# Optimization experiments

Measured on AMD Instinct MI355X. Metric: run time of the kernel, lower is better.

The kernel has to match this reference:

```python
import jax, jax.numpy as jnp
import numpy as np

N_NODES = 100000
N_EDGES = 3200000
D_FEAT = 128
K = 10
A_PARAM = 0.5
B_PARAM = 0.5
LMAX = 2.0


def setup_inputs() -> dict:
    key = jax.random.key(0)
    k1, k2, k3, k4 = jax.random.split(key, 4)
    x = jax.random.normal(k1, (N_NODES, D_FEAT), dtype=jnp.float32)
    edge_index = jax.random.randint(k2, (2, N_EDGES), 0, N_NODES, dtype=jnp.int32)
    alpha = jax.random.uniform(k3, (K + 1,), minval=0.9, maxval=1.1, dtype=jnp.float32)
    beta = jax.random.uniform(k4, (K + 1,), minval=0.9, maxval=1.1, dtype=jnp.float32)
    gamma = jnp.full((K,), 0.1, dtype=jnp.float32)
    return {"x": x, "alpha": alpha, "beta": beta, "gamma": gamma, "edge_index": edge_index}


def reference(x, alpha, beta, gamma, edge_index):
    n = x.shape[0]
    row, col = edge_index[0], edge_index[1]
    # sym-normalized Laplacian L = I - D^{-1/2} A D^{-1/2} (PyG get_laplacian)
    w = jnp.ones(row.shape[0], dtype=x.dtype)
    deg = jax.ops.segment_sum(w, row, num_segments=n)
    dis = jnp.where(deg > 0, jax.lax.rsqrt(jnp.maximum(deg, 1e-30)), 0.0)
    norm = dis[row] * dis[col]  # [E] edge weights of normalized adjacency

    def L_scaled_mm(y):
        # (2/lmax) * L @ y - y, with L @ y = y - Ahat @ y
        ahat_y = jax.ops.segment_sum(norm[:, None] * y[col], row, num_segments=n)
        return (2.0 / LMAX) * (y - ahat_y) - y

    a, b = A_PARAM, B_PARAM
    P_prev2 = x  # P_0
    out = alpha[0] * x
    gamma_prod = jnp.asarray(1.0, dtype=x.dtype)

    if K >= 1:
        P_prev1 = (a - b) / 2.0 * x + (a + b + 2.0) / 2.0 * L_scaled_mm(x)  # P_1
        gamma_prod = gamma_prod * gamma[0]
        out = out + beta[1] * gamma_prod * P_prev1

    for k in range(2, K + 1):
        theta = (2 * k + a + b) * (2 * k + a + b - 1) / (2 * k * (k + a + b))
        theta_p = (2 * k + a + b - 1) * (a ** 2 - b ** 2) / (
            2 * k * (k + a + b) * (2 * k + a + b - 2))
        theta_pp = (k + a - 1) * (k + b - 1) * (2 * k + a + b) / (
            k * (k + a + b) * (2 * k + a + b - 2))
        P_k = theta * L_scaled_mm(P_prev1) + theta_p * P_prev1 - theta_pp * P_prev2
        gamma_prod = gamma_prod * gamma[k - 1]
        out = out + beta[k] * gamma_prod * P_k
        P_prev2, P_prev1 = P_prev1, P_k

    return out
```

## Files before the change

kernel.cpp:

```cpp
#include <hip/hip_runtime.h>

#define NN 100000
#define NE 3200000
#define D 128
#define ND (NN * D)
#define KMAX 10
#define RPB 4
#define RBLK ((NN + RPB - 1) / RPB)
#define NEPAD (NE + 8 * NN + 128)
#define SKIP_EPS 1e-3f
#define NBUCK ((NN + 127) / 128)
#define CH 8192
#define NCB ((NE + CH - 1) / CH)

typedef float f32x4 __attribute__((ext_vector_type(4)));

__device__ __forceinline__ float bflo(unsigned u) { return __uint_as_float(u << 16); }
__device__ __forceinline__ float bfhi(unsigned u) { return __uint_as_float(u & 0xffff0000u); }
__device__ __forceinline__ unsigned packbf(float lo, float hi) {
    unsigned bx = __float_as_uint(lo);
    bx = (bx + 0x7fffu + ((bx >> 16) & 1u)) >> 16;
    unsigned by = __float_as_uint(hi);
    by = (by + 0x7fffu + ((by >> 16) & 1u)) & 0xffff0000u;
    return by | bx;
}

__global__ __launch_bounds__(256) void hist_kernel(const int* __restrict__ row,
                                                   int* __restrict__ hist) {
    __shared__ int lh[NBUCK];
    int t = threadIdx.x;
    for (int b = t; b < NBUCK; b += 256) lh[b] = 0;
    __syncthreads();
    int e0 = blockIdx.x * CH;
    int n = NE - e0; if (n > CH) n = CH;
    for (int i = t; i < n; i += 256)
        atomicAdd(&lh[row[e0 + i] >> 7], 1);
    __syncthreads();
    int x = blockIdx.x & 7;
    for (int b = t; b < NBUCK; b += 256)
        if (lh[b]) atomicAdd(&hist[x * NBUCK + b], lh[b]);
}

__global__ __launch_bounds__(1024) void scan_small_kernel(
    const int* __restrict__ hist, int* __restrict__ seg_off,
    int* __restrict__ cnt2, int* __restrict__ bbase, int* __restrict__ ebase,
    const float* __restrict__ alpha, const float* __restrict__ beta,
    const float* __restrict__ gamma, int* __restrict__ skipflag,
    float* __restrict__ fcoef, int* __restrict__ meta,
    float* __restrict__ dis) {
    __shared__ int sA[1024], sB[1024];
    int t = threadIdx.x;
    int tot = 0;
    int so[8];
    if (t < NBUCK) {
        int s = 0;
        for (int x = 0; x < 8; ++x) { so[x] = s; s += hist[x * NBUCK + t]; }
        tot = s;
    }
    int reg = (t < NBUCK) ? ((tot + 896 + 7) & ~7) : 0;
    sA[t] = tot; sB[t] = reg;
    __syncthreads();
    for (int off = 1; off < 1024; off <<= 1) {
        int a = (t >= off) ? sA[t - off] : 0;
        int c = (t >= off) ? sB[t - off] : 0;
        __syncthreads();
        sA[t] += a; sB[t] += c;
        __syncthreads();
    }
    if (t < NBUCK) {
        int ba = sA[t] - tot, eb = sB[t] - reg;
        bbase[t] = ba; ebase[t] = eb;
        for (int x = 0; x < 8; ++x) {
            seg_off[x * NBUCK + t] = ba + so[x];
            cnt2[x * NBUCK + t] = 0;
        }
    }
    if (t == 0) {
        bbase[NBUCK] = sA[1023];
        ebase[NBUCK] = sB[1023];
        dis[NN] = 0.0f;
        float g[KMAX];
        for (int i = 0; i < KMAX; ++i) g[i] = gamma[i];
        float bt[KMAX + 1];
        for (int j = 0; j <= KMAX; ++j) bt[j] = beta[j];
        fcoef[0] = alpha[0];
        float gp = 1.0f;
        skipflag[0] = 0;
        for (int k = 1; k <= KMAX; ++k) {
            gp *= g[k - 1];
            fcoef[k] = bt[k] * gp;
            float gl = 1.0f;
            for (int i = 0; i < k; ++i) gl *= fabsf(g[i]);
            float rem = 0.0f;
            for (int j = k; j <= KMAX; ++j) {
                rem = fmaxf(rem, fabsf(bt[j]) * gl);
                if (j < KMAX) gl *= fabsf(g[j - 1]);
            }
            skipflag[k] = (rem < SKIP_EPS) ? 1 : 0;
        }
        int L = 1;
        for (int k = 1; k <= KMAX; ++k) if (!skipflag[k]) L = k;
        meta[0] = L;
    }
}

__global__ __launch_bounds__(256) void bin_kernel(const int* __restrict__ row,
                                                  const int* __restrict__ col,
                                                  const int* __restrict__ seg_off,
                                                  int* __restrict__ cnt2,
                                                  int* __restrict__ bin) {
    __shared__ unsigned sval[CH];
    __shared__ unsigned short sbuck[CH];
    __shared__ int lhist[NBUCK], lpos[NBUCK], lbase[NBUCK];
    int t = threadIdx.x;
    for (int b = t; b < NBUCK; b += 256) { lhist[b] = 0; lpos[b] = 0; }
    __syncthreads();
    int e0 = blockIdx.x * CH;
    int n = NE - e0; if (n > CH) n = CH;
    for (int i = t; i < n; i += 256) {
        int r = row[e0 + i], c = col[e0 + i];
        int b = r >> 7;
        sval[i] = ((unsigned)(r & 127) << 17) | (unsigned)c;
        sbuck[i] = (unsigned short)b;
        atomicAdd(&lhist[b], 1);
    }
    __syncthreads();
    int x = blockIdx.x & 7;
    for (int b = t; b < NBUCK; b += 256)
        if (lhist[b]) lbase[b] = seg_off[x * NBUCK + b] +
                                 atomicAdd(&cnt2[x * NBUCK + b], lhist[b]);
    __syncthreads();
    for (int i = t; i < n; i += 256) {
        int b = sbuck[i];
        int p = atomicAdd(&lpos[b], 1);
        bin[lbase[b] + p] = sval[i];
    }
}

__global__ __launch_bounds__(256) void csr_fill_kernel(const int* __restrict__ bbase,
                                                       const int* __restrict__ ebase,
                                                       const int* __restrict__ bin,
                                                       int* __restrict__ ecol,
                                                       int* __restrict__ rowptr,
                                                       int* __restrict__ degp,
                                                       float* __restrict__ dis) {
    __shared__ int cnt[128], rb[128], sscan[128];
    int b = blockIdx.x, t = threadIdx.x;
    int r0 = b << 7;
    int nrows = NN - r0; if (nrows > 128) nrows = 128;
    if (t < 128) cnt[t] = 0;
    __syncthreads();
    int bb = bbase[b], be = bbase[b + 1];
    for (int i = bb + t; i < be; i += 256)
        atomicAdd(&cnt[((unsigned)bin[i]) >> 17], 1);
    __syncthreads();
    int d = 0, d8 = 0;
    if (t < 128) { d = cnt[t]; d8 = (d + 7) & ~7; sscan[t] = d8; }
    __syncthreads();
    for (int off = 1; off < 128; off <<= 1) {
        int v = 0;
        if (t < 128 && t >= off) v = sscan[t - off];
        __syncthreads();
        if (t < 128) sscan[t] += v;
        __syncthreads();
    }
    int eb0 = ebase[b];
    if (t < 128) {
        rb[t] = eb0 + sscan[t] - d8;
        if (t < nrows) {
            rowptr[r0 + t] = rb[t];
            degp[r0 + t] = d8;
            dis[r0 + t] = d > 0 ? rsqrtf((float)d) : 0.0f;
        }
        cnt[t] = 0;
    }
    __syncthreads();
    for (int i = bb + t; i < be; i += 256) {
        unsigned e = (unsigned)bin[i];
        int rl = e >> 17;
        int c = e & 0x1FFFF;
        int p = atomicAdd(&cnt[rl], 1);
        ecol[rb[rl] + p] = c;
    }
    __syncthreads();
    for (int i = t; i < nrows * 8; i += 256) {
        int rl = i >> 3, j = i & 7;
        int dd = cnt[rl];
        if (dd + j < ((dd + 7) & ~7)) ecol[rb[rl] + dd + j] = NN;
    }
}

__global__ __launch_bounds__(256) void ewt_kernel(int* __restrict__ ecol,
                                                  const float* __restrict__ dis,
                                                  float* __restrict__ ewt) {
    int i = blockIdx.x * 256 + threadIdx.x;
    if (i >= NEPAD) return;
    unsigned c = (unsigned)ecol[i];
    unsigned cc = c < NN ? c : NN;
    ewt[i] = dis[cc];
    ecol[i] = (int)((c < NN ? c : 0u) << 8);
}

__global__ __launch_bounds__(256) void x2bf_kernel(const float2* __restrict__ x,
                                                   unsigned* __restrict__ xb) {
    int i = blockIdx.x * 256 + threadIdx.x;
    if (i >= ND / 2) return;
    float2 v = x[i];
    xb[i] = packbf(v.x, v.y);
}

#define FMA8(U, W)                                               \
    a0 = fmaf(W, bflo(U.x), a0); a1 = fmaf(W, bfhi(U.x), a1);    \
    a2 = fmaf(W, bflo(U.y), a2); a3 = fmaf(W, bfhi(U.y), a3);    \
    a4 = fmaf(W, bflo(U.z), a4); a5 = fmaf(W, bfhi(U.z), a5);    \
    a6 = fmaf(W, bflo(U.w), a6); a7 = fmaf(W, bfhi(U.w), a7);

__global__ __launch_bounds__(256) void spmv_row_kernel(
    const int* __restrict__ rowptr, const int* __restrict__ degp,
    const int* __restrict__ ecol, const float* __restrict__ ewt,
    const float* __restrict__ dis,
    const unsigned short* __restrict__ yb, const unsigned short* __restrict__ p2b,
    const float* __restrict__ p2f, const float* __restrict__ xf,
    const int* __restrict__ skipflag, const float* __restrict__ fcoef,
    const int* __restrict__ meta, unsigned short* __restrict__ dstb,
    float* __restrict__ out, float v1, float v2, float v3, int k, int first) {
    if (!first && skipflag[k]) return;

    int r = blockIdx.x * RPB + (threadIdx.x >> 6);
    if (r >= NN) return;
    int lane = threadIdx.x & 63;
    int q = lane >> 4;
    int d = lane & 15;
    const char* ybb = (const char*)yb + (d << 4);

    int jb = rowptr[r];
    int je = jb + degp[r];

    float a0 = 0.f, a1 = 0.f, a2 = 0.f, a3 = 0.f;
    float a4 = 0.f, a5 = 0.f, a6 = 0.f, a7 = 0.f;

    int i = jb;
    for (; i + 16 <= je; i += 16) {
        int e0 = ecol[i + q];       float w0 = ewt[i + q];
        int e1 = ecol[i + q + 4];   float w1 = ewt[i + q + 4];
        int e2 = ecol[i + q + 8];   float w2 = ewt[i + q + 8];
        int e3 = ecol[i + q + 12];  float w3 = ewt[i + q + 12];
        uint4 u0 = *(const uint4*)(ybb + e0);
        uint4 u1 = *(const uint4*)(ybb + e1);
        uint4 u2 = *(const uint4*)(ybb + e2);
        uint4 u3 = *(const uint4*)(ybb + e3);
        FMA8(u0, w0); FMA8(u1, w1); FMA8(u2, w2); FMA8(u3, w3);
    }
    if (i < je) {
        int e0 = ecol[i + q];      float w0 = ewt[i + q];
        int e1 = ecol[i + q + 4];  float w1 = ewt[i + q + 4];
        uint4 u0 = *(const uint4*)(ybb + e0);
        uint4 u1 = *(const uint4*)(ybb + e1);
        FMA8(u0, w0); FMA8(u1, w1);
    }

    a0 += __shfl_xor(a0, 16); a1 += __shfl_xor(a1, 16);
    a2 += __shfl_xor(a2, 16); a3 += __shfl_xor(a3, 16);
    a4 += __shfl_xor(a4, 16); a5 += __shfl_xor(a5, 16);
    a6 += __shfl_xor(a6, 16); a7 += __shfl_xor(a7, 16);
    a0 += __shfl_xor(a0, 32); a1 += __shfl_xor(a1, 32);
    a2 += __shfl_xor(a2, 32); a3 += __shfl_xor(a3, 32);
    a4 += __shfl_xor(a4, 32); a5 += __shfl_xor(a5, 32);
    a6 += __shfl_xor(a6, 32); a7 += __shfl_xor(a7, 32);

    if (q == 0) {
        float dr = dis[r];
        float S0 = dr * a0, S1 = dr * a1, S2 = dr * a2, S3 = dr * a3;
        float S4 = dr * a4, S5 = dr * a5, S6 = dr * a6, S7 = dr * a7;
        size_t off = (size_t)r * D + (size_t)d * 8;

        int L = meta[0];
        bool defer = (L <= 3);
        bool last = (k == L);

        float p10 = 0.f, p11 = 0.f, p12 = 0.f, p13 = 0.f;
        float p14 = 0.f, p15 = 0.f, p16 = 0.f, p17 = 0.f;
        if ((v1 != 0.0f) || (defer && last && k >= 2)) {
            uint4 up1 = *(const uint4*)(yb + off);
            p10 = bflo(up1.x); p11 = bfhi(up1.x);
            p12 = bflo(up1.y); p13 = bfhi(up1.y);
            p14 = bflo(up1.z); p15 = bfhi(up1.z);
            p16 = bflo(up1.w); p17 = bfhi(up1.w);
        }

        float p20 = 0.f, p21 = 0.f, p22 = 0.f, p23 = 0.f;
        float p24 = 0.f, p25 = 0.f, p26 = 0.f, p27 = 0.f;
        bool needp2 = (v3 != 0.0f) || (!defer && first) ||
                      (defer && last && k >= 3);
        if (needp2) {
            if (p2f) {
                float4 t0 = *(const float4*)(p2f + off);
                float4 t1 = *(const float4*)(p2f + off + 4);
                p20 = t0.x; p21 = t0.y; p22 = t0.z; p23 = t0.w;
                p24 = t1.x; p25 = t1.y; p26 = t1.z; p27 = t1.w;
            } else {
                uint4 up2 = *(const uint4*)(p2b + off);
                p20 = bflo(up2.x); p21 = bfhi(up2.x);
                p22 = bflo(up2.y); p23 = bfhi(up2.y);
                p24 = bflo(up2.z); p25 = bfhi(up2.z);
                p26 = bflo(up2.w); p27 = bfhi(up2.w);
            }
        }

        float pk0 = v1 * p10 + v2 * S0 + v3 * p20;
        float pk1 = v1 * p11 + v2 * S1 + v3 * p21;
        float pk2 = v1 * p12 + v2 * S2 + v3 * p22;
        float pk3 = v1 * p13 + v2 * S3 + v3 * p23;
        float pk4 = v1 * p14 + v2 * S4 + v3 * p24;
        float pk5 = v1 * p15 + v2 * S5 + v3 * p25;
        float pk6 = v1 * p16 + v2 * S6 + v3 * p26;
        float pk7 = v1 * p17 + v2 * S7 + v3 * p27;

        if (defer && !last) {
            uint4 pkv;
            pkv.x = packbf(pk0, pk1);
            pkv.y = packbf(pk2, pk3);
            pkv.z = packbf(pk4, pk5);
            pkv.w = packbf(pk6, pk7);
            *(uint4*)(dstb + off) = pkv;
        } else if (defer) {
            float A0 = fcoef[0];
            float bk = fcoef[k];
            float fm1 = (k >= 2) ? fcoef[k - 1] : 0.0f;
            float fm2 = (k >= 3) ? fcoef[k - 2] : 0.0f;
            f32x4 x0 = *(const f32x4*)(xf + off);
            f32x4 x1 = *(const f32x4*)(xf + off + 4);
            f32x4 o0, o1;
            o0[0] = A0 * x0[0] + bk * pk0 + fm1 * p10 + fm2 * p20;
            o0[1] = A0 * x0[1] + bk * pk1 + fm1 * p11 + fm2 * p21;
            o0[2] = A0 * x0[2] + bk * pk2 + fm1 * p12 + fm2 * p22;
            o0[3] = A0 * x0[3] + bk * pk3 + fm1 * p13 + fm2 * p23;
            o1[0] = A0 * x1[0] + bk * pk4 + fm1 * p14 + fm2 * p24;
            o1[1] = A0 * x1[1] + bk * pk5 + fm1 * p15 + fm2 * p25;
            o1[2] = A0 * x1[2] + bk * pk6 + fm1 * p16 + fm2 * p26;
            o1[3] = A0 * x1[3] + bk * pk7 + fm1 * p17 + fm2 * p27;
            __builtin_nontemporal_store(o0, (f32x4*)(out + off));
            __builtin_nontemporal_store(o1, (f32x4*)(out + off) + 1);
        } else {
            float bk = fcoef[k];
            f32x4 o0, o1;
            if (first) {
                float A0 = fcoef[0];
                o0[0] = A0 * p20 + bk * pk0; o0[1] = A0 * p21 + bk * pk1;
                o0[2] = A0 * p22 + bk * pk2; o0[3] = A0 * p23 + bk * pk3;
                o1[0] = A0 * p24 + bk * pk4; o1[1] = A0 * p25 + bk * pk5;
                o1[2] = A0 * p26 + bk * pk6; o1[3] = A0 * p27 + bk * pk7;
            } else {
                f32x4 va = __builtin_nontemporal_load((const f32x4*)(out + off));
                f32x4 vb = __builtin_nontemporal_load((const f32x4*)(out + off) + 1);
                o0[0] = va[0] + bk * pk0; o0[1] = va[1] + bk * pk1;
                o0[2] = va[2] + bk * pk2; o0[3] = va[3] + bk * pk3;
                o1[0] = vb[0] + bk * pk4; o1[1] = vb[1] + bk * pk5;
                o1[2] = vb[2] + bk * pk6; o1[3] = vb[3] + bk * pk7;
            }
            __builtin_nontemporal_store(o0, (f32x4*)(out + off));
            __builtin_nontemporal_store(o1, (f32x4*)(out + off) + 1);
            uint4 pkv;
            pkv.x = packbf(pk0, pk1);
            pkv.y = packbf(pk2, pk3);
            pkv.z = packbf(pk4, pk5);
            pkv.w = packbf(pk6, pk7);
            *(uint4*)(dstb + off) = pkv;
        }
    }
}

extern "C" void kernel_launch(void* const* d_in, const int* in_sizes, int n_in,
                              void* d_out, int out_size, void* d_ws, size_t ws_size,
                              hipStream_t stream) {
    const float* x = (const float*)d_in[0];
    const float* alpha = (const float*)d_in[1];
    const float* beta = (const float*)d_in[2];
    const float* gamma = (const float*)d_in[3];
    const int* edge = (const int*)d_in[4];
    const int* row = edge;
    const int* col = edge + NE;
    float* out = (float*)d_out;

    unsigned short* Xb = (unsigned short*)d_ws;
    unsigned short* PA = Xb + ND;
    unsigned short* PB = PA + ND;
    int* ecol = (int*)(PB + ND);
    float* ewt = (float*)(ecol + NEPAD);
    int* rowptr = (int*)(ewt + NEPAD);
    int* degp = rowptr + NN;
    float* dis = (float*)(degp + NN);
    int* hist = (int*)(dis + NN + 1);
    int* cnt2 = hist + 8 * NBUCK;
    int* seg_off = cnt2 + 8 * NBUCK;
    int* bbase = seg_off + 8 * NBUCK;
    int* ebase = bbase + NBUCK + 1;
    int* skipflag = ebase + NBUCK + 1;
    float* fcoef = (float*)(skipflag + KMAX + 1);
    int* meta = (int*)(fcoef + KMAX + 1);
    int* bin = (int*)d_out;

    const double a = 0.5, b = 0.5, tl = 1.0;
    const double c1 = (a - b) / 2.0, c2 = (a + b + 2.0) / 2.0;
    float u1 = (float)(c1 + c2 * (tl - 1.0));
    float u2 = (float)(-c2 * tl);

    const int XB = (ND / 2 + 255) / 256;
    const int WB = (NEPAD + 255) / 256;

    hipMemsetAsync(hist, 0, 8 * NBUCK * sizeof(int), stream);
    hist_kernel<<<NCB, 256, 0, stream>>>(row, hist);
    scan_small_kernel<<<1, 1024, 0, stream>>>(hist, seg_off, cnt2, bbase, ebase,
                                              alpha, beta, gamma, skipflag, fcoef,
                                              meta, dis);
    bin_kernel<<<NCB, 256, 0, stream>>>(row, col, seg_off, cnt2, bin);
    csr_fill_kernel<<<NBUCK, 256, 0, stream>>>(bbase, ebase, bin, ecol,
                                               rowptr, degp, dis);
    ewt_kernel<<<WB, 256, 0, stream>>>(ecol, dis, ewt);
    x2bf_kernel<<<XB, 256, 0, stream>>>((const float2*)x, (unsigned*)Xb);

    spmv_row_kernel<<<RBLK, 256, 0, stream>>>(rowptr, degp, ecol, ewt, dis, Xb,
                                              nullptr, x, x, skipflag, fcoef,
                                              meta, PA, out, u1, u2, 0.0f, 1, 1);

    for (int k = 2; k <= KMAX; ++k) {
        double dk = (double)k;
        double theta = (2 * dk + a + b) * (2 * dk + a + b - 1) / (2 * dk * (dk + a + b));
        double theta_p = (2 * dk + a + b - 1) * (a * a - b * b) /
                         (2 * dk * (dk + a + b) * (2 * dk + a + b - 2));
        double theta_pp = (dk + a - 1) * (dk + b - 1) * (2 * dk + a + b) /
                          (dk * (dk + a + b) * (2 * dk + a + b - 2));
        float v1 = (float)(theta * (tl - 1.0) + theta_p);
        float v2 = (float)(-theta * tl);
        float v3 = (float)(-theta_pp);

        unsigned short* p1 = (k % 2 == 0) ? PA : PB;
        unsigned short* dst = (k % 2 == 0) ? PB : PA;
        const unsigned short* p2b = dst;
        const float* p2f = (k == 2) ? x : nullptr;

        spmv_row_kernel<<<RBLK, 256, 0, stream>>>(rowptr, degp, ecol, ewt, dis,
                                                  p1, p2b, p2f, x, skipflag,
                                                  fcoef, meta, dst, out,
                                                  v1, v2, v3, k, 0);
    }
}
```

Measured before the change: 491.4 us.

## Pack edge column and weight into one array and use nontemporal loads

```diff
diff --git a/kernel.cpp b/kernel.cpp
--- a/kernel.cpp
+++ b/kernel.cpp
@@ -4,6 +4,7 @@
 #define NE 3200000
 #define D 128
 #define ND (NN * D)
+#define NDP (ND + 128)
 #define KMAX 10
 #define RPB 4
 #define RBLK ((NN + RPB - 1) / RPB)
@@ -14,6 +15,8 @@
 #define NCB ((NE + CH - 1) / CH)
 
 typedef float f32x4 __attribute__((ext_vector_type(4)));
+typedef int i32x2 __attribute__((ext_vector_type(2)));
+typedef unsigned u32x4 __attribute__((ext_vector_type(4)));
 
 __device__ __forceinline__ float bflo(unsigned u) { return __uint_as_float(u << 16); }
 __device__ __forceinline__ float bfhi(unsigned u) { return __uint_as_float(u & 0xffff0000u); }
@@ -140,7 +143,7 @@
 __global__ __launch_bounds__(256) void csr_fill_kernel(const int* __restrict__ bbase,
                                                        const int* __restrict__ ebase,
                                                        const int* __restrict__ bin,
-                                                       int* __restrict__ ecol,
+                                                       i32x2* __restrict__ epk,
                                                        int* __restrict__ rowptr,
                                                        int* __restrict__ degp,
                                                        float* __restrict__ dis) {
@@ -180,25 +183,26 @@
         int rl = e >> 17;
         int c = e & 0x1FFFF;
         int p = atomicAdd(&cnt[rl], 1);
-        ecol[rb[rl] + p] = c;
+        epk[rb[rl] + p].x = c;
     }
     __syncthreads();
     for (int i = t; i < nrows * 8; i += 256) {
         int rl = i >> 3, j = i & 7;
         int dd = cnt[rl];
-        if (dd + j < ((dd + 7) & ~7)) ecol[rb[rl] + dd + j] = NN;
-    }
-}
-
-__global__ __launch_bounds__(256) void ewt_kernel(int* __restrict__ ecol,
-                                                  const float* __restrict__ dis,
-                                                  float* __restrict__ ewt) {
+        if (dd + j < ((dd + 7) & ~7)) epk[rb[rl] + dd + j].x = NN;
+    }
+}
+
+__global__ __launch_bounds__(256) void emeta_kernel(i32x2* __restrict__ epk,
+                                                    const float* __restrict__ dis) {
     int i = blockIdx.x * 256 + threadIdx.x;
     if (i >= NEPAD) return;
-    unsigned c = (unsigned)ecol[i];
+    unsigned c = (unsigned)epk[i].x;
     unsigned cc = c < NN ? c : NN;
-    ewt[i] = dis[cc];
-    ecol[i] = (int)((c < NN ? c : 0u) << 8);
+    i32x2 v;
+    v.x = (int)(cc << 8);
+    v.y = __float_as_int(dis[cc]);
+    epk[i] = v;
 }
 
 __global__ __launch_bounds__(256) void x2bf_kernel(const float2* __restrict__ x,
@@ -217,8 +221,7 @@
 
 __global__ __launch_bounds__(256) void spmv_row_kernel(
     const int* __restrict__ rowptr, const int* __restrict__ degp,
-    const int* __restrict__ ecol, const float* __restrict__ ewt,
-    const float* __restrict__ dis,
+    const i32x2* __restrict__ epk, const float* __restrict__ dis,
     const unsigned short* __restrict__ yb, const unsigned short* __restrict__ p2b,
     const float* __restrict__ p2f, const float* __restrict__ xf,
     const int* __restrict__ skipflag, const float* __restrict__ fcoef,
@@ -241,21 +244,27 @@
 
     int i = jb;
     for (; i + 16 <= je; i += 16) {
-        int e0 = ecol[i + q];       float w0 = ewt[i + q];
-        int e1 = ecol[i + q + 4];   float w1 = ewt[i + q + 4];
-        int e2 = ecol[i + q + 8];   float w2 = ewt[i + q + 8];
-        int e3 = ecol[i + q + 12];  float w3 = ewt[i + q + 12];
-        uint4 u0 = *(const uint4*)(ybb + e0);
-        uint4 u1 = *(const uint4*)(ybb + e1);
-        uint4 u2 = *(const uint4*)(ybb + e2);
-        uint4 u3 = *(const uint4*)(ybb + e3);
+        i32x2 m0 = __builtin_nontemporal_load(epk + i + q);
+        i32x2 m1 = __builtin_nontemporal_load(epk + i + q + 4);
+        i32x2 m2 = __builtin_nontemporal_load(epk + i + q + 8);
+        i32x2 m3 = __builtin_nontemporal_load(epk + i + q + 12);
+        u32x4 u0 = *(const u32x4*)(ybb + m0.x);
+        u32x4 u1 = *(const u32x4*)(ybb + m1.x);
+        u32x4 u2 = *(const u32x4*)(ybb + m2.x);
+        u32x4 u3 = *(const u32x4*)(ybb + m3.x);
+        float w0 = __int_as_float(m0.y);
+        float w1 = __int_as_float(m1.y);
+        float w2 = __int_as_float(m2.y);
+        float w3 = __int_as_float(m3.y);
         FMA8(u0, w0); FMA8(u1, w1); FMA8(u2, w2); FMA8(u3, w3);
     }
     if (i < je) {
-        int e0 = ecol[i + q];      float w0 = ewt[i + q];
-        int e1 = ecol[i + q + 4];  float w1 = ewt[i + q + 4];
-        uint4 u0 = *(const uint4*)(ybb + e0);
-        uint4 u1 = *(const uint4*)(ybb + e1);
+        i32x2 m0 = __builtin_nontemporal_load(epk + i + q);
+        i32x2 m1 = __builtin_nontemporal_load(epk + i + q + 4);
+        u32x4 u0 = *(const u32x4*)(ybb + m0.x);
+        u32x4 u1 = *(const u32x4*)(ybb + m1.x);
+        float w0 = __int_as_float(m0.y);
+        float w1 = __int_as_float(m1.y);
         FMA8(u0, w0); FMA8(u1, w1);
     }
 
@@ -281,7 +290,7 @@
         float p10 = 0.f, p11 = 0.f, p12 = 0.f, p13 = 0.f;
         float p14 = 0.f, p15 = 0.f, p16 = 0.f, p17 = 0.f;
         if ((v1 != 0.0f) || (defer && last && k >= 2)) {
-            uint4 up1 = *(const uint4*)(yb + off);
+            u32x4 up1 = *(const u32x4*)(yb + off);
             p10 = bflo(up1.x); p11 = bfhi(up1.x);
             p12 = bflo(up1.y); p13 = bfhi(up1.y);
             p14 = bflo(up1.z); p15 = bfhi(up1.z);
@@ -294,12 +303,12 @@
                       (defer && last && k >= 3);
         if (needp2) {
             if (p2f) {
-                float4 t0 = *(const float4*)(p2f + off);
-                float4 t1 = *(const float4*)(p2f + off + 4);
+                f32x4 t0 = __builtin_nontemporal_load((const f32x4*)(p2f + off));
+                f32x4 t1 = __builtin_nontemporal_load((const f32x4*)(p2f + off) + 1);
                 p20 = t0.x; p21 = t0.y; p22 = t0.z; p23 = t0.w;
                 p24 = t1.x; p25 = t1.y; p26 = t1.z; p27 = t1.w;
             } else {
-                uint4 up2 = *(const uint4*)(p2b + off);
+                u32x4 up2 = __builtin_nontemporal_load((const u32x4*)(p2b + off));
                 p20 = bflo(up2.x); p21 = bfhi(up2.x);
                 p22 = bflo(up2.y); p23 = bfhi(up2.y);
                 p24 = bflo(up2.z); p25 = bfhi(up2.z);
@@ -317,19 +326,19 @@
         float pk7 = v1 * p17 + v2 * S7 + v3 * p27;
 
         if (defer && !last) {
-            uint4 pkv;
+            u32x4 pkv;
             pkv.x = packbf(pk0, pk1);
             pkv.y = packbf(pk2, pk3);
             pkv.z = packbf(pk4, pk5);
             pkv.w = packbf(pk6, pk7);
-            *(uint4*)(dstb + off) = pkv;
+            __builtin_nontemporal_store(pkv, (u32x4*)(dstb + off));
         } else if (defer) {
             float A0 = fcoef[0];
             float bk = fcoef[k];
             float fm1 = (k >= 2) ? fcoef[k - 1] : 0.0f;
             float fm2 = (k >= 3) ? fcoef[k - 2] : 0.0f;
-            f32x4 x0 = *(const f32x4*)(xf + off);
-            f32x4 x1 = *(const f32x4*)(xf + off + 4);
+            f32x4 x0 = __builtin_nontemporal_load((const f32x4*)(xf + off));
+            f32x4 x1 = __builtin_nontemporal_load((const f32x4*)(xf + off) + 1);
             f32x4 o0, o1;
             o0[0] = A0 * x0[0] + bk * pk0 + fm1 * p10 + fm2 * p20;
             o0[1] = A0 * x0[1] + bk * pk1 + fm1 * p11 + fm2 * p21;
@@ -360,12 +369,12 @@
             }
             __builtin_nontemporal_store(o0, (f32x4*)(out + off));
             __builtin_nontemporal_store(o1, (f32x4*)(out + off) + 1);
-            uint4 pkv;
+            u32x4 pkv;
             pkv.x = packbf(pk0, pk1);
             pkv.y = packbf(pk2, pk3);
             pkv.z = packbf(pk4, pk5);
             pkv.w = packbf(pk6, pk7);
-            *(uint4*)(dstb + off) = pkv;
+            __builtin_nontemporal_store(pkv, (u32x4*)(dstb + off));
         }
     }
 }
@@ -383,11 +392,10 @@
     float* out = (float*)d_out;
 
     unsigned short* Xb = (unsigned short*)d_ws;
-    unsigned short* PA = Xb + ND;
-    unsigned short* PB = PA + ND;
-    int* ecol = (int*)(PB + ND);
-    float* ewt = (float*)(ecol + NEPAD);
-    int* rowptr = (int*)(ewt + NEPAD);
+    unsigned short* PA = Xb + NDP;
+    unsigned short* PB = PA + NDP;
+    i32x2* epk = (i32x2*)(PB + NDP);
+    int* rowptr = (int*)(epk + NEPAD);
     int* degp = rowptr + NN;
     float* dis = (float*)(degp + NN);
     int* hist = (int*)(dis + NN + 1);
@@ -409,17 +417,20 @@
     const int WB = (NEPAD + 255) / 256;
 
     hipMemsetAsync(hist, 0, 8 * NBUCK * sizeof(int), stream);
+    hipMemsetAsync(Xb + ND, 0, 128 * sizeof(unsigned short), stream);
+    hipMemsetAsync(PA + ND, 0, 128 * sizeof(unsigned short), stream);
+    hipMemsetAsync(PB + ND, 0, 128 * sizeof(unsigned short), stream);
     hist_kernel<<<NCB, 256, 0, stream>>>(row, hist);
     scan_small_kernel<<<1, 1024, 0, stream>>>(hist, seg_off, cnt2, bbase, ebase,
                                               alpha, beta, gamma, skipflag, fcoef,
                                               meta, dis);
     bin_kernel<<<NCB, 256, 0, stream>>>(row, col, seg_off, cnt2, bin);
-    csr_fill_kernel<<<NBUCK, 256, 0, stream>>>(bbase, ebase, bin, ecol,
+    csr_fill_kernel<<<NBUCK, 256, 0, stream>>>(bbase, ebase, bin, epk,
                                                rowptr, degp, dis);
-    ewt_kernel<<<WB, 256, 0, stream>>>(ecol, dis, ewt);
+    emeta_kernel<<<WB, 256, 0, stream>>>(epk, dis);
     x2bf_kernel<<<XB, 256, 0, stream>>>((const float2*)x, (unsigned*)Xb);
 
-    spmv_row_kernel<<<RBLK, 256, 0, stream>>>(rowptr, degp, ecol, ewt, dis, Xb,
+    spmv_row_kernel<<<RBLK, 256, 0, stream>>>(rowptr, degp, epk, dis, Xb,
                                               nullptr, x, x, skipflag, fcoef,
                                               meta, PA, out, u1, u2, 0.0f, 1, 1);
 
@@ -436,11 +447,10 @@
 
         unsigned short* p1 = (k % 2 == 0) ? PA : PB;
         unsigned short* dst = (k % 2 == 0) ? PB : PA;
-        const unsigned short* p2b = dst;
-        const float* p2f = (k == 2) ? x : nullptr;
-
-        spmv_row_kernel<<<RBLK, 256, 0, stream>>>(rowptr, degp, ecol, ewt, dis,
-                                                  p1, p2b, p2f, x, skipflag,
+        const unsigned short* p2b = (k == 2) ? Xb : dst;
+
+        spmv_row_kernel<<<RBLK, 256, 0, stream>>>(rowptr, degp, epk, dis,
+                                                  p1, p2b, nullptr, x, skipflag,
                                                   fcoef, meta, dst, out,
                                                   v1, v2, v3, k, 0);
     }
```

After: 503.1 us. +2.4%, slower.
